# Optimization experiments

Hardware: AMD Instinct MI355X
Metric: run time of the kernel (lower is better)

## Reference

```python
import jax, jax.numpy as jnp
import numpy as np

L, D, H, FF = 4, 256, 8, 4 * 256  # num_layers, d_model, nhead, ffn hidden
DK = D // H
EPS = 1e-5


def _ln(x, g, b):
    mu = jnp.mean(x, axis=-1, keepdims=True)
    var = jnp.mean(jnp.square(x - mu), axis=-1, keepdims=True)
    return (x - mu) * jax.lax.rsqrt(var + EPS) * g + b


def setup_inputs() -> dict:
    key = jax.random.key(0)
    ks = jax.random.split(key, 16)
    B, N = 8, 1024
    s = 0.02
    return {
        "x": jax.random.normal(ks[0], (B, N, D), jnp.float32),
        "coords": jax.random.normal(ks[1], (B, N, 3), jnp.float32),
        "Wq": jax.random.normal(ks[2], (L, D, D), jnp.float32) * s,
        "bq": jnp.zeros((L, D), jnp.float32),
        "Wk": jax.random.normal(ks[3], (L, D, D), jnp.float32) * s,
        "bk": jnp.zeros((L, D), jnp.float32),
        "Wv": jax.random.normal(ks[4], (L, D, D), jnp.float32) * s,
        "bv": jnp.zeros((L, D), jnp.float32),
        "alpha": jnp.full((L,), 0.1, jnp.float32),
        "W1": jax.random.normal(ks[5], (L, D, FF), jnp.float32) * s,
        "b1": jnp.zeros((L, FF), jnp.float32),
        "W2": jax.random.normal(ks[6], (L, FF, D), jnp.float32) * s,
        "b2": jnp.zeros((L, D), jnp.float32),
        "g1": jnp.ones((L, D), jnp.float32),
        "be1": jnp.zeros((L, D), jnp.float32),
        "g2": jnp.ones((L, D), jnp.float32),
        "be2": jnp.zeros((L, D), jnp.float32),
    }


def reference(x, coords, Wq, bq, Wk, bk, Wv, bv, alpha, W1, b1, W2, b2, g1, be1, g2, be2):
    B, N, _ = x.shape
    # Per-batch pairwise coord dot products (same math as the BN x BN matmul
    # sliced per batch in the original, computed without the cross-batch waste).
    G0 = jnp.einsum("bnc,bmc->bnm", coords, coords)  # [B,N,N]
    scale = 1.0 / jnp.sqrt(jnp.float32(DK))
    for i in range(L):
        q = (x @ Wq[i] + bq[i]).reshape(B, N, H, DK)
        k = (x @ Wk[i] + bk[i]).reshape(B, N, H, DK)
        v = (x @ Wv[i] + bv[i]).reshape(B, N, H, DK)
        scores = jnp.einsum("bnhd,bmhd->bhnm", q, k) * scale + (alpha[i] * G0)[:, None]
        attn = jax.nn.softmax(scores, axis=-1)
        out = jnp.einsum("bhnm,bmhd->bnhd", attn, v).reshape(B, N, D)
        x = _ln(x + out, g1[i], be1[i])
        ff = jnp.maximum(x @ W1[i] + b1[i], 0.0) @ W2[i] + b2[i]
        x = _ln(x + ff, g2[i], be2[i])
    return x
```

## Files before the change

kernel.cpp:

```cpp
#include <hip/hip_runtime.h>
#include <hip/hip_bf16.h>

#define BB 8
#define NN 1024
#define DD 256
#define HH 8
#define DK 32
#define FFN 1024
#define NLAYERS 4
#define MM (BB * NN)
#define ROW_ELEMS (MM * DD)

#define QSCALE 0.2550655192922103f
#define LOG2E  1.4426950408889634f

typedef unsigned short ushort_t;
typedef __attribute__((ext_vector_type(8))) short bf16x8;
typedef __attribute__((ext_vector_type(4))) short bf16x4;
typedef __attribute__((ext_vector_type(4))) float f32x4;

__device__ __forceinline__ f32x4 mfma16(bf16x4 a, bf16x4 b, f32x4 c) {
#if __has_builtin(__builtin_amdgcn_mfma_f32_16x16x16bf16_1k)
    return __builtin_amdgcn_mfma_f32_16x16x16bf16_1k(a, b, c, 0, 0, 0);
#elif defined(__AMDGCN__)
    f32x4 d;
    asm volatile("v_mfma_f32_16x16x16_bf16 %0, %1, %2, %3"
                 : "=v"(d)
                 : "v"(a), "v"(b), "v"(c));
    return d;
#else
    return c;
#endif
}

__device__ __forceinline__ ushort_t f2b(float f) {
    __hip_bfloat16 h = __float2bfloat16(f);
    return *reinterpret_cast<ushort_t*>(&h);
}

__device__ __forceinline__ float fast_exp2(float x) {
#if __has_builtin(__builtin_amdgcn_exp2f)
    return __builtin_amdgcn_exp2f(x);
#else
    return exp2f(x);
#endif
}

__device__ __forceinline__ void async_ld16(const void* g, void* l) {
    __builtin_amdgcn_global_load_lds((const __attribute__((address_space(1))) void*)g,
                                     (__attribute__((address_space(3))) void*)l, 16, 0, 0);
}

__global__ __launch_bounds__(256) void copy_in_kernel(const float4* __restrict__ in,
                                                      float4* __restrict__ xf,
                                                      ushort4* __restrict__ xb, int n4) {
    int i = blockIdx.x * 256 + threadIdx.x;
    if (i < n4) {
        float4 v = in[i];
        xf[i] = v;
        ushort4 b = {f2b(v.x), f2b(v.y), f2b(v.z), f2b(v.w)};
        xb[i] = b;
    }
}

__global__ __launch_bounds__(256) void qkext_init_kernel(const float* __restrict__ coords,
                                                         ushort_t* __restrict__ Qa,
                                                         ushort_t* __restrict__ Ka) {
    const int id = blockIdx.x * 256 + threadIdx.x;
    const int bh = id >> 10, n = id & 1023;
    const int b = bh >> 3;
    ushort_t buf[32];
#pragma unroll
    for (int d = 0; d < 32; ++d) buf[d] = 0;
    buf[0] = f2b(coords[(size_t)(b * NN + n) * 3 + 0]);
    buf[1] = f2b(coords[(size_t)(b * NN + n) * 3 + 1]);
    buf[2] = f2b(coords[(size_t)(b * NN + n) * 3 + 2]);
    ushort_t* kp = Ka + ((size_t)bh * NN + n) * 64 + 32;
    ushort_t* qp = Qa + ((size_t)bh * NN + n) * 64 + 32;
    const uint4* b4 = (const uint4*)buf;
    uint4 z4 = {0u, 0u, 0u, 0u};
#pragma unroll
    for (int c = 0; c < 4; ++c) {
        *(uint4*)(kp + c * 8) = b4[c];
        *(uint4*)(qp + c * 8) = z4;
    }
}

__global__ __launch_bounds__(256) void prep_kernel(const float* __restrict__ Wq,
                                                   const float* __restrict__ Wk,
                                                   const float* __restrict__ Wv,
                                                   const float* __restrict__ W1,
                                                   const float* __restrict__ W2,
                                                   const float* __restrict__ bq,
                                                   const float* __restrict__ bk,
                                                   const float* __restrict__ bv,
                                                   ushort_t* __restrict__ wqkvt,
                                                   ushort_t* __restrict__ w1t,
                                                   ushort_t* __restrict__ w2t,
                                                   float* __restrict__ bqkv) {
    const int id = blockIdx.x;
    const int layer = id / 707;
    const int r = id % 707;
    const int tid = threadIdx.x;

    if (r >= 704) {
        const int chunk = r - 704;
        const float* src = (chunk == 0) ? bq : (chunk == 1) ? bk : bv;
        bqkv[layer * 768 + chunk * 256 + tid] = src[layer * 256 + tid];
        return;
    }

    const float* src;
    ushort_t* dst;
    int R, C, x, y;
    if (r < 192) {
        const int w = r >> 6, rr = r & 63;
        src = ((w == 0) ? Wq : (w == 1) ? Wk : Wv) + (size_t)layer * 65536;
        dst = wqkvt + (size_t)layer * 196608 + w * 65536;
        R = 256; C = 256; x = rr & 7; y = rr >> 3;
    } else if (r < 448) {
        const int rr = r - 192;
        src = W1 + (size_t)layer * 262144;
        dst = w1t + (size_t)layer * 262144;
        R = 256; C = 1024; x = rr & 31; y = rr >> 5;
    } else {
        const int rr = r - 448;
        src = W2 + (size_t)layer * 262144;
        dst = w2t + (size_t)layer * 262144;
        R = 1024; C = 256; x = rr & 7; y = rr >> 3;
    }
    const int r0 = y * 32, c0 = x * 32;
    __shared__ float tile[32][33];
    const int tx = tid & 31, ty = tid >> 5;
#pragma unroll
    for (int i = 0; i < 4; ++i)
        tile[ty + 8 * i][tx] = src[(size_t)(r0 + ty + 8 * i) * C + (c0 + tx)];
    __syncthreads();
#pragma unroll
    for (int i = 0; i < 4; ++i)
        dst[(size_t)(c0 + ty + 8 * i) * R + (r0 + tx)] = f2b(tile[tx][ty + 8 * i]);
}

template <int MODE, int BM>
__global__ __launch_bounds__(256) void mfma_gemm_kernel(const ushort_t* __restrict__ A,
                                                        const ushort_t* __restrict__ Bt,
                                                        const float* __restrict__ bias,
                                                        void* __restrict__ C0,
                                                        void* __restrict__ C1,
                                                        void* __restrict__ C2,
                                                        const float* __restrict__ coords,
                                                        const float* __restrict__ alpha, int layer,
                                                        int K, int ldc) {
    constexpr int NI = BM / 32;
    __shared__ ushort_t As0[2][BM * 32];
    __shared__ ushort_t As1[2][BM * 32];
    __shared__ ushort_t Bs0[2][128 * 32];
    __shared__ ushort_t Bs1[2][128 * 32];

    const int t    = threadIdx.x;
    const int bm   = blockIdx.y * BM;
    const int bn   = blockIdx.x * 128;
    const int wave = t >> 6, lane = t & 63;
    const int wm   = (wave >> 1) * (BM / 2), wn = (wave & 1) * 64;
    const int quad = lane >> 4, l16 = lane & 15;

    const int srow = t >> 2;
    const int scol = (t & 3) * 8;

    f32x4 acc[NI][4];
#pragma unroll
    for (int i = 0; i < NI; ++i)
#pragma unroll
        for (int j = 0; j < 4; ++j) {
            f32x4 z = {0.f, 0.f, 0.f, 0.f};
            acc[i][j] = z;
        }

    auto stage = [&](int pb, int k0) {
        async_ld16(A + (size_t)(bm + srow) * K + k0 + scol, As0[pb] + wave * 512);
        if constexpr (BM == 128)
            async_ld16(A + (size_t)(bm + 64 + srow) * K + k0 + scol, As0[pb] + 2048 + wave * 512);
        async_ld16(Bt + (size_t)(bn + srow) * K + k0 + scol, Bs0[pb] + wave * 512);
        async_ld16(Bt + (size_t)(bn + 64 + srow) * K + k0 + scol, Bs0[pb] + 2048 + wave * 512);
        async_ld16(A + (size_t)(bm + srow) * K + k0 + 32 + scol, As1[pb] + wave * 512);
        if constexpr (BM == 128)
            async_ld16(A + (size_t)(bm + 64 + srow) * K + k0 + 32 + scol, As1[pb] + 2048 + wave * 512);
        async_ld16(Bt + (size_t)(bn + srow) * K + k0 + 32 + scol, Bs1[pb] + wave * 512);
        async_ld16(Bt + (size_t)(bn + 64 + srow) * K + k0 + 32 + scol, Bs1[pb] + 2048 + wave * 512);
    };

    stage(0, 0);
    int pb = 0;
    for (int k0 = 0; k0 < K; k0 += 64, pb ^= 1) {
        __syncthreads();

        if (k0 + 64 < K) stage(pb ^ 1, k0 + 64);

        bf16x8 af0[NI], af1[NI], bf0[4], bf1[4];
#pragma unroll
        for (int i = 0; i < NI; ++i) {
            af0[i] = *(const bf16x8*)(As0[pb] + (wm + i * 16 + l16) * 32 + quad * 8);
            af1[i] = *(const bf16x8*)(As1[pb] + (wm + i * 16 + l16) * 32 + quad * 8);
        }
#pragma unroll
        for (int j = 0; j < 4; ++j) {
            bf0[j] = *(const bf16x8*)(Bs0[pb] + (wn + j * 16 + l16) * 32 + quad * 8);
            bf1[j] = *(const bf16x8*)(Bs1[pb] + (wn + j * 16 + l16) * 32 + quad * 8);
        }
#pragma unroll
        for (int i = 0; i < NI; ++i)
#pragma unroll
            for (int j = 0; j < 4; ++j) {
                acc[i][j] = __builtin_amdgcn_mfma_f32_16x16x32_bf16(af0[i], bf0[j], acc[i][j], 0, 0, 0);
                acc[i][j] = __builtin_amdgcn_mfma_f32_16x16x32_bf16(af1[i], bf1[j], acc[i][j], 0, 0, 0);
            }
    }

    const float av = (MODE == 2) ? alpha[layer] : 0.f;

#pragma unroll
    for (int j = 0; j < 4; ++j) {
        const int col = bn + wn + j * 16 + l16;
        const float bsv = bias[col];
#pragma unroll
        for (int i = 0; i < NI; ++i) {
            const int row0 = bm + wm + i * 16 + quad * 4;
            if (MODE == 2) {
                const int bb2 = row0 >> 10, nn0 = row0 & 1023;
                const int which = col >> 8, rem = col & 255;
                const int h = rem >> 5, d = rem & 31;
                const size_t bh = (size_t)((bb2 << 3) + h);
                if (which == 2) {
                    ushort4 pk;
                    pk.x = f2b(acc[i][j][0] + bsv);
                    pk.y = f2b(acc[i][j][1] + bsv);
                    pk.z = f2b(acc[i][j][2] + bsv);
                    pk.w = f2b(acc[i][j][3] + bsv);
                    *(ushort4*)&((ushort_t*)C2)[(bh * DK + d) * NN + nn0] = pk;
                } else {
#pragma unroll
                    for (int r = 0; r < 4; ++r) {
                        const float v = acc[i][j][r] + bsv;
                        const int nn = nn0 + r;
                        if (which == 0) {
                            ((ushort_t*)C0)[(bh * NN + nn) * 64 + d] = f2b(v * QSCALE);
                            if (d < 3)
                                ((ushort_t*)C0)[(bh * NN + nn) * 64 + 32 + d] =
                                    f2b(av * LOG2E * coords[(size_t)(bb2 * NN + nn) * 3 + d]);
                        } else {
                            ((ushort_t*)C1)[(bh * NN + nn) * 64 + d] = f2b(v);
                        }
                    }
                }
            } else {
#pragma unroll
                for (int r = 0; r < 4; ++r) {
                    float v = acc[i][j][r] + bsv;
                    if (MODE == 0)
                        ((float*)C0)[(size_t)(row0 + r) * ldc + col] = v;
                    else
                        ((ushort_t*)C0)[(size_t)(row0 + r) * ldc + col] = f2b(fmaxf(v, 0.f));
                }
            }
        }
    }
}

__global__ __launch_bounds__(512) void ffn_ln_kernel(const ushort_t* __restrict__ A,
                                                     const ushort_t* __restrict__ W1t,
                                                     const ushort_t* __restrict__ W2t,
                                                     const float* __restrict__ b1,
                                                     const float* __restrict__ b2,
                                                     const float* __restrict__ xres,
                                                     const float* __restrict__ g,
                                                     const float* __restrict__ be,
                                                     float* __restrict__ xout,
                                                     ushort_t* __restrict__ xb) {
    __shared__ ushort_t Ha[32][32][32];
    __shared__ ushort_t Asf[8][32][32];
    __shared__ ushort_t Bs0[2][256 * 32];
    __shared__ ushort_t Bs1[2][256 * 32];
    __shared__ float redS[8][32];
    __shared__ float redQ[8][32];

    const int t = threadIdx.x;
    const int bm = blockIdx.x * 32;
    const int wave = t >> 6, lane = t & 63;
    const int quad = lane >> 4, l16 = lane & 15;
    const int wn = wave * 32;
    const int scol = (t & 3) * 8;

#pragma unroll
    for (int c = 0; c < 2; ++c) {
        const int arow = (t >> 2) & 31;
        const int acol = (c * 4 + (t >> 7)) * 32 + scol;
        async_ld16(A + (size_t)(bm + arow) * 256 + acol,
                   (ushort_t*)Asf + c * 4096 + wave * 512);
    }

    auto stageB1 = [&](int pb, int step) {
        const int nbase = (step >> 2) * 256;
        const int k0 = (step & 3) * 64;
#pragma unroll
        for (int c = 0; c < 2; ++c) {
            const int brow = nbase + c * 128 + (t >> 2);
            async_ld16(W1t + (size_t)brow * 256 + k0 + scol, Bs0[pb] + c * 4096 + wave * 512);
            async_ld16(W1t + (size_t)brow * 256 + k0 + 32 + scol, Bs1[pb] + c * 4096 + wave * 512);
        }
    };
    auto stageB2 = [&](int pb, int step) {
        const int k0 = step * 64;
#pragma unroll
        for (int c = 0; c < 2; ++c) {
            const int brow = c * 128 + (t >> 2);
            async_ld16(W2t + (size_t)brow * 1024 + k0 + scol, Bs0[pb] + c * 4096 + wave * 512);
            async_ld16(W2t + (size_t)brow * 1024 + k0 + 32 + scol, Bs1[pb] + c * 4096 + wave * 512);
        }
    };

    f32x4 acc1[2][2], acc2[2][2];
#pragma unroll
    for (int i = 0; i < 2; ++i)
#pragma unroll
        for (int j = 0; j < 2; ++j) {
            f32x4 z = {0.f, 0.f, 0.f, 0.f};
            acc1[i][j] = z;
            acc2[i][j] = z;
        }

    stageB1(0, 0);
    int pb = 0;

    for (int step = 0; step < 16; ++step, pb ^= 1) {
        __syncthreads();
        if (step < 15) stageB1(pb ^ 1, step + 1);
        else stageB2(pb ^ 1, 0);

        const int ks = step & 3;
        bf16x8 af0[2], af1[2], bf0[2], bf1[2];
#pragma unroll
        for (int i = 0; i < 2; ++i) {
            af0[i] = *(const bf16x8*)&Asf[2 * ks][i * 16 + l16][quad * 8];
            af1[i] = *(const bf16x8*)&Asf[2 * ks + 1][i * 16 + l16][quad * 8];
        }
#pragma unroll
        for (int j = 0; j < 2; ++j) {
            bf0[j] = *(const bf16x8*)(Bs0[pb] + (wn + j * 16 + l16) * 32 + quad * 8);
            bf1[j] = *(const bf16x8*)(Bs1[pb] + (wn + j * 16 + l16) * 32 + quad * 8);
        }
#pragma unroll
        for (int i = 0; i < 2; ++i)
#pragma unroll
            for (int j = 0; j < 2; ++j) {
                acc1[i][j] = __builtin_amdgcn_mfma_f32_16x16x32_bf16(af0[i], bf0[j], acc1[i][j], 0, 0, 0);
                acc1[i][j] = __builtin_amdgcn_mfma_f32_16x16x32_bf16(af1[i], bf1[j], acc1[i][j], 0, 0, 0);
            }

        if (ks == 3) {
            const int nc = step >> 2;
#pragma unroll
            for (int j = 0; j < 2; ++j) {
                const int col = nc * 256 + wn + j * 16 + l16;
                const float bj = b1[col];
#pragma unroll
                for (int i = 0; i < 2; ++i)
#pragma unroll
                    for (int r = 0; r < 4; ++r) {
                        const int row = i * 16 + quad * 4 + r;
                        Ha[nc * 8 + wave][row][j * 16 + l16] =
                            f2b(fmaxf(acc1[i][j][r] + bj, 0.f));
                    }
            }
#pragma unroll
            for (int i = 0; i < 2; ++i)
#pragma unroll
                for (int j = 0; j < 2; ++j) {
                    f32x4 z = {0.f, 0.f, 0.f, 0.f};
                    acc1[i][j] = z;
                }
        }
    }

    for (int step = 0; step < 16; ++step, pb ^= 1) {
        __syncthreads();
        if (step < 15) stageB2(pb ^ 1, step + 1);

        bf16x8 af0[2], af1[2], bf0[2], bf1[2];
#pragma unroll
        for (int i = 0; i < 2; ++i) {
            af0[i] = *(const bf16x8*)&Ha[2 * step][i * 16 + l16][quad * 8];
            af1[i] = *(const bf16x8*)&Ha[2 * step + 1][i * 16 + l16][quad * 8];
        }
#pragma unroll
        for (int j = 0; j < 2; ++j) {
            bf0[j] = *(const bf16x8*)(Bs0[pb] + (wn + j * 16 + l16) * 32 + quad * 8);
            bf1[j] = *(const bf16x8*)(Bs1[pb] + (wn + j * 16 + l16) * 32 + quad * 8);
        }
#pragma unroll
        for (int i = 0; i < 2; ++i)
#pragma unroll
            for (int j = 0; j < 2; ++j) {
                acc2[i][j] = __builtin_amdgcn_mfma_f32_16x16x32_bf16(af0[i], bf0[j], acc2[i][j], 0, 0, 0);
                acc2[i][j] = __builtin_amdgcn_mfma_f32_16x16x32_bf16(af1[i], bf1[j], acc2[i][j], 0, 0, 0);
            }
    }

    float mean[2][4], rstd[2][4];

    {
        float sum_[2][4];
#pragma unroll
        for (int i = 0; i < 2; ++i)
#pragma unroll
            for (int r = 0; r < 4; ++r) sum_[i][r] = 0.f;
#pragma unroll
        for (int j = 0; j < 2; ++j) {
            const int col = wn + j * 16 + l16;
            const float bj = b2[col];
#pragma unroll
            for (int i = 0; i < 2; ++i) {
                const int row = bm + i * 16 + quad * 4;
#pragma unroll
                for (int r = 0; r < 4; ++r) {
                    const float v = acc2[i][j][r] + bj + xres[(size_t)(row + r) * DD + col];
                    acc2[i][j][r] = v;
                    sum_[i][r] += v;
                }
            }
        }
#pragma unroll
        for (int i = 0; i < 2; ++i)
#pragma unroll
            for (int r = 0; r < 4; ++r) {
                float s = sum_[i][r];
                s += __shfl_xor(s, 1);
                s += __shfl_xor(s, 2);
                s += __shfl_xor(s, 4);
                s += __shfl_xor(s, 8);
                sum_[i][r] = s;
            }
        if (l16 == 0) {
#pragma unroll
            for (int i = 0; i < 2; ++i)
#pragma unroll
                for (int r = 0; r < 4; ++r) redS[wave][i * 16 + quad * 4 + r] = sum_[i][r];
        }
        __syncthreads();
#pragma unroll
        for (int i = 0; i < 2; ++i)
#pragma unroll
            for (int r = 0; r < 4; ++r) {
                const int rl = i * 16 + quad * 4 + r;
                float s = 0.f;
#pragma unroll
                for (int w = 0; w < 8; ++w) s += redS[w][rl];
                mean[i][r] = s * (1.0f / 256.0f);
            }
    }

    {
        float sq_[2][4];
#pragma unroll
        for (int i = 0; i < 2; ++i)
#pragma unroll
            for (int r = 0; r < 4; ++r) sq_[i][r] = 0.f;
#pragma unroll
        for (int j = 0; j < 2; ++j)
#pragma unroll
            for (int i = 0; i < 2; ++i)
#pragma unroll
                for (int r = 0; r < 4; ++r) {
                    const float d = acc2[i][j][r] - mean[i][r];
                    sq_[i][r] += d * d;
                }
#pragma unroll
        for (int i = 0; i < 2; ++i)
#pragma unroll
            for (int r = 0; r < 4; ++r) {
                float s = sq_[i][r];
                s += __shfl_xor(s, 1);
                s += __shfl_xor(s, 2);
                s += __shfl_xor(s, 4);
                s += __shfl_xor(s, 8);
                sq_[i][r] = s;
            }
        if (l16 == 0) {
#pragma unroll
            for (int i = 0; i < 2; ++i)
#pragma unroll
                for (int r = 0; r < 4; ++r) redQ[wave][i * 16 + quad * 4 + r] = sq_[i][r];
        }
        __syncthreads();
#pragma unroll
        for (int i = 0; i < 2; ++i)
#pragma unroll
            for (int r = 0; r < 4; ++r) {
                const int rl = i * 16 + quad * 4 + r;
                float s = 0.f;
#pragma unroll
                for (int w = 0; w < 8; ++w) s += redQ[w][rl];
                rstd[i][r] = rsqrtf(s * (1.0f / 256.0f) + 1e-5f);
            }
    }

#pragma unroll
    for (int j = 0; j < 2; ++j) {
        const int col = wn + j * 16 + l16;
        const float gv = g[col];
        const float bev = be[col];
#pragma unroll
        for (int i = 0; i < 2; ++i) {
            const int row = bm + i * 16 + quad * 4;
#pragma unroll
            for (int r = 0; r < 4; ++r) {
                const float y = (acc2[i][j][r] - mean[i][r]) * rstd[i][r] * gv + bev;
                xout[(size_t)(row + r) * DD + col] = y;
                xb[(size_t)(row + r) * DD + col] = f2b(y);
            }
        }
    }
}

__global__ __launch_bounds__(256, 2) void attn8_kernel(const ushort_t* __restrict__ Qa,
                                                       const ushort_t* __restrict__ Ka,
                                                       const ushort_t* __restrict__ Vt,
                                                       float* __restrict__ aout) {
    const int b = blockIdx.x, h = blockIdx.y, n0 = blockIdx.z * 64;
    const int t = threadIdx.x, wave = t >> 6, lane = t & 63;
    const int quad = lane >> 4, l16 = lane & 15;
    const int bh = b * HH + h;

    __shared__ __align__(16) char smem[56320];
    ushort_t (*Ks)[64][72] = (ushort_t (*)[64][72])smem;
    ushort_t (*Vs)[32][72] = (ushort_t (*)[32][72])(smem + 36864);
    float    (*Om)[64][36] = (float (*)[64][36])smem;
    float    (*Lm)[64]     = (float (*)[64])(smem + 55296);

    bf16x8 aq[4][2];
#pragma unroll
    for (int s = 0; s < 4; ++s) {
        const ushort_t* qp = Qa + ((size_t)bh * NN + n0 + s * 16 + l16) * 64 + quad * 8;
        aq[s][0] = *(const bf16x8*)qp;
        aq[s][1] = *(const bf16x8*)(qp + 32);
    }

    const f32x4 z = {0.f, 0.f, 0.f, 0.f};
    f32x4 acc[4][2];
    float lsum[4];
#pragma unroll
    for (int s = 0; s < 4; ++s) { acc[s][0] = z; acc[s][1] = z; lsum[s] = 0.f; }

    const ushort_t* kg = Ka + ((size_t)bh * NN + wave * 256) * 64;
    const ushort_t* vg = Vt + (size_t)bh * DK * NN + wave * 256;

    const int srow = lane >> 3, sch = (lane & 7) * 8;

    uint4 kreg[8], vreg[4];
#pragma unroll
    for (int i = 0; i < 8; ++i) kreg[i] = *(const uint4*)(kg + (size_t)(i * 8 + srow) * 64 + sch);
#pragma unroll
    for (int i = 0; i < 4; ++i) vreg[i] = *(const uint4*)(vg + (size_t)(i * 8 + srow) * NN + sch);

    for (int kt = 0; kt < 4; ++kt) {
#pragma unroll
        for (int i = 0; i < 8; ++i) *(uint4*)&Ks[wave][i * 8 + srow][sch] = kreg[i];
#pragma unroll
        for (int i = 0; i < 4; ++i) *(uint4*)&Vs[wave][i * 8 + srow][sch] = vreg[i];

        bf16x8 bk0[4], bk1[4];
#pragma unroll
        for (int jt = 0; jt < 4; ++jt) {
            bk0[jt] = *(const bf16x8*)&Ks[wave][jt * 16 + l16][quad * 8];
            bk1[jt] = *(const bf16x8*)&Ks[wave][jt * 16 + l16][32 + quad * 8];
        }
        bf16x4 vfrag[2][4];
#pragma unroll
        for (int g = 0; g < 2; ++g)
#pragma unroll
            for (int jt = 0; jt < 4; ++jt)
                vfrag[g][jt] = *(const bf16x4*)&Vs[wave][g * 16 + l16][jt * 16 + quad * 4];

        if (kt < 3) {
            const ushort_t* kg2 = kg + (size_t)(kt + 1) * 64 * 64;
            const ushort_t* vg2 = vg + (kt + 1) * 64;
#pragma unroll
            for (int i = 0; i < 8; ++i)
                kreg[i] = *(const uint4*)(kg2 + (size_t)(i * 8 + srow) * 64 + sch);
#pragma unroll
            for (int i = 0; i < 4; ++i)
                vreg[i] = *(const uint4*)(vg2 + (size_t)(i * 8 + srow) * NN + sch);
        }

#pragma unroll
        for (int s = 0; s < 4; ++s) {
            f32x4 st[4];
            __builtin_amdgcn_s_setprio(1);
#pragma unroll
            for (int jt = 0; jt < 4; ++jt) {
                st[jt] = __builtin_amdgcn_mfma_f32_16x16x32_bf16(bk0[jt], aq[s][0], z, 0, 0, 0);
                st[jt] = __builtin_amdgcn_mfma_f32_16x16x32_bf16(bk1[jt], aq[s][1], st[jt], 0, 0, 0);
            }
            __builtin_amdgcn_s_setprio(0);
            bf16x4 pf[4];
            float ls = 0.f;
#pragma unroll
            for (int jt = 0; jt < 4; ++jt) {
                float e0 = fast_exp2(st[jt][0]);
                float e1 = fast_exp2(st[jt][1]);
                float e2 = fast_exp2(st[jt][2]);
                float e3 = fast_exp2(st[jt][3]);
                ls += (e0 + e1) + (e2 + e3);
                pf[jt][0] = (short)f2b(e0);
                pf[jt][1] = (short)f2b(e1);
                pf[jt][2] = (short)f2b(e2);
                pf[jt][3] = (short)f2b(e3);
            }
            lsum[s] += ls;
            __builtin_amdgcn_s_setprio(1);
#pragma unroll
            for (int jt = 0; jt < 4; ++jt) {
                acc[s][0] = mfma16(vfrag[0][jt], pf[jt], acc[s][0]);
                acc[s][1] = mfma16(vfrag[1][jt], pf[jt], acc[s][1]);
            }
            __builtin_amdgcn_s_setprio(0);
        }
    }

#pragma unroll
    for (int s = 0; s < 4; ++s) {
        lsum[s] += __shfl_xor(lsum[s], 16);
        lsum[s] += __shfl_xor(lsum[s], 32);
    }

    __syncthreads();
    if (quad == 0) {
#pragma unroll
        for (int s = 0; s < 4; ++s) Lm[wave][s * 16 + l16] = lsum[s];
    }

#pragma unroll
    for (int s = 0; s < 4; ++s) {
        const int q = s * 16 + l16;
#pragma unroll
        for (int g = 0; g < 2; ++g) {
            float4 v = {acc[s][g][0], acc[s][g][1], acc[s][g][2], acc[s][g][3]};
            *(float4*)&Om[wave][q][g * 16 + quad * 4] = v;
        }
    }
    __syncthreads();

    {
        const int q = t >> 2, dseg = (t & 3) * 8;
        const float inv = 1.0f / (Lm[0][q] + Lm[1][q] + Lm[2][q] + Lm[3][q]);
        float* op = aout + (size_t)(b * NN + n0 + q) * DD + h * DK + dseg;
        float4 s0 = {0.f, 0.f, 0.f, 0.f}, s1 = {0.f, 0.f, 0.f, 0.f};
#pragma unroll
        for (int w = 0; w < 4; ++w) {
            float4 a = *(const float4*)&Om[w][q][dseg];
            float4 c = *(const float4*)&Om[w][q][dseg + 4];
            s0.x += a.x; s0.y += a.y; s0.z += a.z; s0.w += a.w;
            s1.x += c.x; s1.y += c.y; s1.z += c.z; s1.w += c.w;
        }
        float4 o0 = {s0.x * inv, s0.y * inv, s0.z * inv, s0.w * inv};
        float4 o1 = {s1.x * inv, s1.y * inv, s1.z * inv, s1.w * inv};
        *(float4*)op = o0;
        *(float4*)(op + 4) = o1;
    }
}

__global__ __launch_bounds__(256) void addln_kernel(const float* __restrict__ x,
                                                    ushort_t* __restrict__ xb,
                                                    const float* __restrict__ delta, int dstride,
                                                    const float* __restrict__ g,
                                                    const float* __restrict__ be,
                                                    float* __restrict__ xout) {
    const int row  = blockIdx.x * 4 + (threadIdx.x >> 6);
    const int lane = threadIdx.x & 63;
    const size_t base = (size_t)row * DD + lane * 4;

    float4 xv = *(const float4*)(x + base);
    float4 dl = *(const float4*)(delta + (size_t)row * dstride + lane * 4);
    float v0 = xv.x + dl.x, v1 = xv.y + dl.y, v2 = xv.z + dl.z, v3 = xv.w + dl.w;

    float s = v0 + v1 + v2 + v3;
#pragma unroll
    for (int off = 32; off; off >>= 1) s += __shfl_xor(s, off);
    const float mean = s * (1.0f / 256.0f);

    float d0 = v0 - mean, d1 = v1 - mean, d2 = v2 - mean, d3 = v3 - mean;
    float s2 = d0 * d0 + d1 * d1 + d2 * d2 + d3 * d3;
#pragma unroll
    for (int off = 32; off; off >>= 1) s2 += __shfl_xor(s2, off);
    const float rs = rsqrtf(s2 * (1.0f / 256.0f) + 1e-5f);

    float4 gv = *(const float4*)(g + lane * 4);
    float4 bv = *(const float4*)(be + lane * 4);
    float y0 = d0 * rs * gv.x + bv.x;
    float y1 = d1 * rs * gv.y + bv.y;
    float y2 = d2 * rs * gv.z + bv.z;
    float y3 = d3 * rs * gv.w + bv.w;

    float4 o = {y0, y1, y2, y3};
    *(float4*)(xout + base) = o;
    ushort4 ob = {f2b(y0), f2b(y1), f2b(y2), f2b(y3)};
    *(ushort4*)(xb + base) = ob;
}

extern "C" void kernel_launch(void* const* d_in, const int* in_sizes, int n_in,
                              void* d_out, int out_size, void* d_ws, size_t ws_size,
                              hipStream_t stream) {
    const float* x      = (const float*)d_in[0];
    const float* coords = (const float*)d_in[1];
    const float* Wq     = (const float*)d_in[2];
    const float* bq     = (const float*)d_in[3];
    const float* Wk     = (const float*)d_in[4];
    const float* bk     = (const float*)d_in[5];
    const float* Wv     = (const float*)d_in[6];
    const float* bv     = (const float*)d_in[7];
    const float* alpha  = (const float*)d_in[8];
    const float* W1     = (const float*)d_in[9];
    const float* b1     = (const float*)d_in[10];
    const float* W2     = (const float*)d_in[11];
    const float* b2     = (const float*)d_in[12];
    const float* g1     = (const float*)d_in[13];
    const float* be1    = (const float*)d_in[14];
    const float* g2     = (const float*)d_in[15];
    const float* be2    = (const float*)d_in[16];

    float* ws = (float*)d_ws;
    float*    xf    = ws;
    ushort_t* xb    = (ushort_t*)(ws + 2097152);
    ushort_t* Qa    = (ushort_t*)(ws + 3145728);
    ushort_t* Ka    = (ushort_t*)(ws + 5242880);
    ushort_t* Vt    = (ushort_t*)(ws + 7340032);
    float*    aout  = ws + 8388608;
    ushort_t* wqkvt = (ushort_t*)(ws + 10485760);
    ushort_t* w1t   = (ushort_t*)(ws + 10878976);
    ushort_t* w2t   = (ushort_t*)(ws + 11403264);
    float*    bqkv  = ws + 11927552;

    prep_kernel<<<NLAYERS * 707, 256, 0, stream>>>(Wq, Wk, Wv, W1, W2, bq, bk, bv,
                                                   wqkvt, w1t, w2t, bqkv);

    copy_in_kernel<<<ROW_ELEMS / 4 / 256, 256, 0, stream>>>((const float4*)x, (float4*)xf,
                                                            (ushort4*)xb, ROW_ELEMS / 4);

    qkext_init_kernel<<<256, 256, 0, stream>>>(coords, Qa, Ka);

    for (int i = 0; i < NLAYERS; ++i) {
        mfma_gemm_kernel<2, 64><<<dim3(6, 128), 256, 0, stream>>>(
            xb, wqkvt + (size_t)i * 196608, bqkv + i * 768, Qa, Ka, Vt,
            coords, alpha, i, 256, 0);

        attn8_kernel<<<dim3(8, 8, 16), 256, 0, stream>>>(Qa, Ka, Vt, aout);

        addln_kernel<<<MM / 4, 256, 0, stream>>>(xf, xb, aout, 256, g1 + i * 256, be1 + i * 256, xf);

        ffn_ln_kernel<<<MM / 32, 512, 0, stream>>>(
            xb, w1t + (size_t)i * 262144, w2t + (size_t)i * 262144,
            b1 + i * 1024, b2 + i * 256, xf,
            g2 + i * 256, be2 + i * 256,
            (i == NLAYERS - 1) ? (float*)d_out : xf, xb);
    }
}
```

Before: 396.6 us.

## Fuse attention with residual add and LayerNorm, one wave per head

Replaces the attention kernel and the separate add+LayerNorm kernel with one kernel. Each 512-thread block handles 32 query rows of one batch, with one wave per head looping over all 1024 keys. This removes the cross-wave key-split reduction and the aout round trip through global memory, and the LayerNorm statistics are reduced across heads in shared memory. In exchange the grid shrinks from 1024 blocks to 256, and each wave runs a 16-step serial loop over keys with fewer query rows per wave, so there is less parallelism and less reuse of each K/V tile.

Result: slower. 644.9 us (+62.6%).

```diff
diff --git a/kernel.cpp b/kernel.cpp
--- a/kernel.cpp
+++ b/kernel.cpp
@@ -521,37 +521,41 @@
     }
 }
 
-__global__ __launch_bounds__(256, 2) void attn8_kernel(const ushort_t* __restrict__ Qa,
-                                                       const ushort_t* __restrict__ Ka,
-                                                       const ushort_t* __restrict__ Vt,
-                                                       float* __restrict__ aout) {
-    const int b = blockIdx.x, h = blockIdx.y, n0 = blockIdx.z * 64;
+__global__ __launch_bounds__(512) void attn_ln_kernel(const ushort_t* __restrict__ Qa,
+                                                      const ushort_t* __restrict__ Ka,
+                                                      const ushort_t* __restrict__ Vt,
+                                                      const float* __restrict__ xres,
+                                                      const float* __restrict__ g,
+                                                      const float* __restrict__ be,
+                                                      float* __restrict__ xout,
+                                                      ushort_t* __restrict__ xb) {
+    const int b = blockIdx.x, n0 = blockIdx.y * 32;
     const int t = threadIdx.x, wave = t >> 6, lane = t & 63;
     const int quad = lane >> 4, l16 = lane & 15;
+    const int h = wave;
     const int bh = b * HH + h;
 
-    __shared__ __align__(16) char smem[56320];
-    ushort_t (*Ks)[64][72] = (ushort_t (*)[64][72])smem;
-    ushort_t (*Vs)[32][72] = (ushort_t (*)[32][72])(smem + 36864);
-    float    (*Om)[64][36] = (float (*)[64][36])smem;
-    float    (*Lm)[64]     = (float (*)[64])(smem + 55296);
-
-    bf16x8 aq[4][2];
-#pragma unroll
-    for (int s = 0; s < 4; ++s) {
+    __shared__ ushort_t Ks[8][64][72];
+    __shared__ ushort_t Vs[8][32][72];
+    __shared__ float redS[8][32];
+    __shared__ float redQ[8][32];
+
+    bf16x8 aq[2][2];
+#pragma unroll
+    for (int s = 0; s < 2; ++s) {
         const ushort_t* qp = Qa + ((size_t)bh * NN + n0 + s * 16 + l16) * 64 + quad * 8;
         aq[s][0] = *(const bf16x8*)qp;
         aq[s][1] = *(const bf16x8*)(qp + 32);
     }
 
     const f32x4 z = {0.f, 0.f, 0.f, 0.f};
-    f32x4 acc[4][2];
-    float lsum[4];
-#pragma unroll
-    for (int s = 0; s < 4; ++s) { acc[s][0] = z; acc[s][1] = z; lsum[s] = 0.f; }
-
-    const ushort_t* kg = Ka + ((size_t)bh * NN + wave * 256) * 64;
-    const ushort_t* vg = Vt + (size_t)bh * DK * NN + wave * 256;
+    f32x4 acc[2][2];
+    float lsum[2];
+#pragma unroll
+    for (int s = 0; s < 2; ++s) { acc[s][0] = z; acc[s][1] = z; lsum[s] = 0.f; }
+
+    const ushort_t* kg = Ka + (size_t)bh * NN * 64;
+    const ushort_t* vg = Vt + (size_t)bh * DK * NN;
 
     const int srow = lane >> 3, sch = (lane & 7) * 8;
 
@@ -561,7 +565,7 @@
 #pragma unroll
     for (int i = 0; i < 4; ++i) vreg[i] = *(const uint4*)(vg + (size_t)(i * 8 + srow) * NN + sch);
 
-    for (int kt = 0; kt < 4; ++kt) {
+    for (int kt = 0; kt < 16; ++kt) {
 #pragma unroll
         for (int i = 0; i < 8; ++i) *(uint4*)&Ks[wave][i * 8 + srow][sch] = kreg[i];
 #pragma unroll
@@ -575,12 +579,12 @@
         }
         bf16x4 vfrag[2][4];
 #pragma unroll
-        for (int g = 0; g < 2; ++g)
+        for (int gg = 0; gg < 2; ++gg)
 #pragma unroll
             for (int jt = 0; jt < 4; ++jt)
-                vfrag[g][jt] = *(const bf16x4*)&Vs[wave][g * 16 + l16][jt * 16 + quad * 4];
-
-        if (kt < 3) {
+                vfrag[gg][jt] = *(const bf16x4*)&Vs[wave][gg * 16 + l16][jt * 16 + quad * 4];
+
+        if (kt < 15) {
             const ushort_t* kg2 = kg + (size_t)(kt + 1) * 64 * 64;
             const ushort_t* vg2 = vg + (kt + 1) * 64;
 #pragma unroll
@@ -592,7 +596,7 @@
         }
 
 #pragma unroll
-        for (int s = 0; s < 4; ++s) {
+        for (int s = 0; s < 2; ++s) {
             f32x4 st[4];
             __builtin_amdgcn_s_setprio(1);
 #pragma unroll
@@ -626,84 +630,97 @@
         }
     }
 
-#pragma unroll
-    for (int s = 0; s < 4; ++s) {
+    float inv[2];
+#pragma unroll
+    for (int s = 0; s < 2; ++s) {
         lsum[s] += __shfl_xor(lsum[s], 16);
         lsum[s] += __shfl_xor(lsum[s], 32);
-    }
-
-    __syncthreads();
-    if (quad == 0) {
-#pragma unroll
-        for (int s = 0; s < 4; ++s) Lm[wave][s * 16 + l16] = lsum[s];
-    }
-
-#pragma unroll
-    for (int s = 0; s < 4; ++s) {
-        const int q = s * 16 + l16;
-#pragma unroll
-        for (int g = 0; g < 2; ++g) {
-            float4 v = {acc[s][g][0], acc[s][g][1], acc[s][g][2], acc[s][g][3]};
-            *(float4*)&Om[wave][q][g * 16 + quad * 4] = v;
-        }
-    }
-    __syncthreads();
+        inv[s] = 1.0f / lsum[s];
+    }
+
+    const int browbase = b * NN + n0;
+    float v[2][2][4];
+    float mean[2], rstd[2];
 
     {
-        const int q = t >> 2, dseg = (t & 3) * 8;
-        const float inv = 1.0f / (Lm[0][q] + Lm[1][q] + Lm[2][q] + Lm[3][q]);
-        float* op = aout + (size_t)(b * NN + n0 + q) * DD + h * DK + dseg;
-        float4 s0 = {0.f, 0.f, 0.f, 0.f}, s1 = {0.f, 0.f, 0.f, 0.f};
-#pragma unroll
-        for (int w = 0; w < 4; ++w) {
-            float4 a = *(const float4*)&Om[w][q][dseg];
-            float4 c = *(const float4*)&Om[w][q][dseg + 4];
-            s0.x += a.x; s0.y += a.y; s0.z += a.z; s0.w += a.w;
-            s1.x += c.x; s1.y += c.y; s1.z += c.z; s1.w += c.w;
-        }
-        float4 o0 = {s0.x * inv, s0.y * inv, s0.z * inv, s0.w * inv};
-        float4 o1 = {s1.x * inv, s1.y * inv, s1.z * inv, s1.w * inv};
-        *(float4*)op = o0;
-        *(float4*)(op + 4) = o1;
-    }
-}
-
-__global__ __launch_bounds__(256) void addln_kernel(const float* __restrict__ x,
-                                                    ushort_t* __restrict__ xb,
-                                                    const float* __restrict__ delta, int dstride,
-                                                    const float* __restrict__ g,
-                                                    const float* __restrict__ be,
-                                                    float* __restrict__ xout) {
-    const int row  = blockIdx.x * 4 + (threadIdx.x >> 6);
-    const int lane = threadIdx.x & 63;
-    const size_t base = (size_t)row * DD + lane * 4;
-
-    float4 xv = *(const float4*)(x + base);
-    float4 dl = *(const float4*)(delta + (size_t)row * dstride + lane * 4);
-    float v0 = xv.x + dl.x, v1 = xv.y + dl.y, v2 = xv.z + dl.z, v3 = xv.w + dl.w;
-
-    float s = v0 + v1 + v2 + v3;
-#pragma unroll
-    for (int off = 32; off; off >>= 1) s += __shfl_xor(s, off);
-    const float mean = s * (1.0f / 256.0f);
-
-    float d0 = v0 - mean, d1 = v1 - mean, d2 = v2 - mean, d3 = v3 - mean;
-    float s2 = d0 * d0 + d1 * d1 + d2 * d2 + d3 * d3;
-#pragma unroll
-    for (int off = 32; off; off >>= 1) s2 += __shfl_xor(s2, off);
-    const float rs = rsqrtf(s2 * (1.0f / 256.0f) + 1e-5f);
-
-    float4 gv = *(const float4*)(g + lane * 4);
-    float4 bv = *(const float4*)(be + lane * 4);
-    float y0 = d0 * rs * gv.x + bv.x;
-    float y1 = d1 * rs * gv.y + bv.y;
-    float y2 = d2 * rs * gv.z + bv.z;
-    float y3 = d3 * rs * gv.w + bv.w;
-
-    float4 o = {y0, y1, y2, y3};
-    *(float4*)(xout + base) = o;
-    ushort4 ob = {f2b(y0), f2b(y1), f2b(y2), f2b(y3)};
-    *(ushort4*)(xb + base) = ob;
+        float sum_[2] = {0.f, 0.f};
+#pragma unroll
+        for (int s = 0; s < 2; ++s) {
+            const size_t row = (size_t)(browbase + s * 16 + l16);
+#pragma unroll
+            for (int gg = 0; gg < 2; ++gg) {
+                const int col = h * DK + gg * 16 + quad * 4;
+                float4 xv = *(const float4*)(xres + row * DD + col);
+                v[s][gg][0] = acc[s][gg][0] * inv[s] + xv.x;
+                v[s][gg][1] = acc[s][gg][1] * inv[s] + xv.y;
+                v[s][gg][2] = acc[s][gg][2] * inv[s] + xv.z;
+                v[s][gg][3] = acc[s][gg][3] * inv[s] + xv.w;
+                sum_[s] += (v[s][gg][0] + v[s][gg][1]) + (v[s][gg][2] + v[s][gg][3]);
+            }
+        }
+#pragma unroll
+        for (int s = 0; s < 2; ++s) {
+            float ss = sum_[s];
+            ss += __shfl_xor(ss, 16);
+            ss += __shfl_xor(ss, 32);
+            if (quad == 0) redS[wave][s * 16 + l16] = ss;
+        }
+        __syncthreads();
+#pragma unroll
+        for (int s = 0; s < 2; ++s) {
+            float m = 0.f;
+#pragma unroll
+            for (int w = 0; w < 8; ++w) m += redS[w][s * 16 + l16];
+            mean[s] = m * (1.0f / 256.0f);
+        }
+    }
+
+    {
+        float sq_[2] = {0.f, 0.f};
+#pragma unroll
+        for (int s = 0; s < 2; ++s)
+#pragma unroll
+            for (int gg = 0; gg < 2; ++gg)
+#pragma unroll
+                for (int r = 0; r < 4; ++r) {
+                    const float d = v[s][gg][r] - mean[s];
+                    sq_[s] += d * d;
+                }
+#pragma unroll
+        for (int s = 0; s < 2; ++s) {
+            float ss = sq_[s];
+            ss += __shfl_xor(ss, 16);
+            ss += __shfl_xor(ss, 32);
+            if (quad == 0) redQ[wave][s * 16 + l16] = ss;
+        }
+        __syncthreads();
+#pragma unroll
+        for (int s = 0; s < 2; ++s) {
+            float q = 0.f;
+#pragma unroll
+            for (int w = 0; w < 8; ++w) q += redQ[w][s * 16 + l16];
+            rstd[s] = rsqrtf(q * (1.0f / 256.0f) + 1e-5f);
+        }
+    }
+
+#pragma unroll
+    for (int s = 0; s < 2; ++s) {
+        const size_t row = (size_t)(browbase + s * 16 + l16);
+#pragma unroll
+        for (int gg = 0; gg < 2; ++gg) {
+            const int col = h * DK + gg * 16 + quad * 4;
+            float4 gv = *(const float4*)(g + col);
+            float4 bv = *(const float4*)(be + col);
+            float y0 = (v[s][gg][0] - mean[s]) * rstd[s] * gv.x + bv.x;
+            float y1 = (v[s][gg][1] - mean[s]) * rstd[s] * gv.y + bv.y;
+            float y2 = (v[s][gg][2] - mean[s]) * rstd[s] * gv.z + bv.z;
+            float y3 = (v[s][gg][3] - mean[s]) * rstd[s] * gv.w + bv.w;
+            float4 o = {y0, y1, y2, y3};
+            *(float4*)(xout + row * DD + col) = o;
+            ushort4 ob = {f2b(y0), f2b(y1), f2b(y2), f2b(y3)};
+            *(ushort4*)(xb + row * DD + col) = ob;
+        }
+    }
 }
 
 extern "C" void kernel_launch(void* const* d_in, const int* in_sizes, int n_in,
@@ -733,7 +750,6 @@
     ushort_t* Qa    = (ushort_t*)(ws + 3145728);
     ushort_t* Ka    = (ushort_t*)(ws + 5242880);
     ushort_t* Vt    = (ushort_t*)(ws + 7340032);
-    float*    aout  = ws + 8388608;
     ushort_t* wqkvt = (ushort_t*)(ws + 10485760);
     ushort_t* w1t   = (ushort_t*)(ws + 10878976);
     ushort_t* w2t   = (ushort_t*)(ws + 11403264);
@@ -752,9 +768,8 @@
             xb, wqkvt + (size_t)i * 196608, bqkv + i * 768, Qa, Ka, Vt,
             coords, alpha, i, 256, 0);
 
-        attn8_kernel<<<dim3(8, 8, 16), 256, 0, stream>>>(Qa, Ka, Vt, aout);
-
-        addln_kernel<<<MM / 4, 256, 0, stream>>>(xf, xb, aout, 256, g1 + i * 256, be1 + i * 256, xf);
+        attn_ln_kernel<<<dim3(8, 32), 512, 0, stream>>>(
+            Qa, Ka, Vt, xf, g1 + i * 256, be1 + i * 256, xf, xb);
 
         ffn_ln_kernel<<<MM / 32, 512, 0, stream>>>(
             xb, w1t + (size_t)i * 262144, w2t + (size_t)i * 262144,
```
